# Performance work log

Measured on AMD Instinct MI355X. Metric: run time of the kernel, lower is better.

The kernel has to match this reference:

```python
import jax, jax.numpy as jnp
import numpy as np

Z, Y, X = 32, 480, 480          # sparse voxel grid (LiDAR-scale)
N = 200_000                     # active voxels
C_IN, C_OUT = 64, 64
EPS = 1e-5


def _subm_conv(f, nbr, w):
    """Submanifold sparse conv as gather-matmul-accumulate.
    f: [N, Cin]; nbr: [N, K] neighbor row ids, pad index == N for missing;
    w: [K, Cin, Cout]."""
    f_pad = jnp.concatenate([f, jnp.zeros((1, f.shape[1]), f.dtype)], axis=0)
    g = f_pad[nbr]                       # [N, K, Cin] gathered neighbor features
    return jnp.einsum('nkc,kco->no', g, w)


def _bn(x, gamma, beta):
    # BatchNorm1d in training mode: batch stats over the N dimension
    m = x.mean(axis=0)
    v = x.var(axis=0)
    return (x - m) * jax.lax.rsqrt(v + EPS) * gamma + beta


def setup_inputs() -> dict:
    rng = np.random.default_rng(0)
    ids = rng.choice(Z * Y * X, size=N, replace=False)
    lookup = np.full(Z * Y * X, -1, dtype=np.int64)
    lookup[ids] = np.arange(N)
    z = ids // (Y * X)
    y = (ids // X) % Y
    x = ids % X

    def nbr_table(offsets):
        cols = []
        for dz, dy, dx in offsets:
            zz, yy, xx = z + dz, y + dy, x + dx
            ok = (zz >= 0) & (zz < Z) & (yy >= 0) & (yy < Y) & (xx >= 0) & (xx < X)
            lin = np.clip((zz * Y + yy) * X + xx, 0, Z * Y * X - 1)
            idx = np.where(ok, lookup[lin], -1)
            cols.append(np.where(idx >= 0, idx, N))   # pad index N -> zero row
        return jnp.asarray(np.stack(cols, axis=1).astype(np.int32))

    off13 = [(0, dy, dx) for dy in (-1, 0, 1) for dx in (-1, 0, 1)]  # kernel (1,3,3)
    off31 = [(dz, 0, dx) for dz in (-1, 0, 1) for dx in (-1, 0, 1)]  # kernel (3,1,3)

    key = jax.random.key(0)
    ks = jax.random.split(key, 5)
    s = 0.05
    ones = jnp.ones((C_OUT,), jnp.float32)
    zeros = jnp.zeros((C_OUT,), jnp.float32)
    return {
        'features': jax.random.normal(ks[0], (N, C_IN), jnp.float32),
        'w1':   jax.random.normal(ks[1], (9, C_IN, C_OUT), jnp.float32) * s,
        'w1_2': jax.random.normal(ks[2], (9, C_OUT, C_OUT), jnp.float32) * s,
        'w2':   jax.random.normal(ks[3], (9, C_IN, C_OUT), jnp.float32) * s,
        'w3':   jax.random.normal(ks[4], (9, C_OUT, C_OUT), jnp.float32) * s,
        'g0': ones, 'b0': zeros, 'g0_2': ones, 'b0_2': zeros,
        'g1': ones, 'b1': zeros, 'g2': ones, 'b2': zeros,
        'nbr13': nbr_table(off13),
        'nbr31': nbr_table(off31),
    }


def reference(features, w1, w1_2, w2, w3, g0, b0, g0_2, b0_2, g1, b1, g2, b2,
              nbr13, nbr31):
    # shortcut branch: conv1x3 -> LeakyReLU -> BN -> conv3x1 -> LeakyReLU -> BN
    sc = _subm_conv(features, nbr13, w1)
    sc = _bn(jax.nn.leaky_relu(sc), g0, b0)
    sc = _subm_conv(sc, nbr31, w1_2)
    sc = _bn(jax.nn.leaky_relu(sc), g0_2, b0_2)
    # main branch: conv3x1 -> LeakyReLU -> BN -> conv1x3 -> LeakyReLU -> BN
    r = _subm_conv(features, nbr31, w2)
    r = _bn(jax.nn.leaky_relu(r), g1, b1)
    r = _subm_conv(r, nbr13, w3)
    r = _bn(jax.nn.leaky_relu(r), g2, b2)
    return r + sc
```

## Files before the change

kernel.cpp:

```cpp
#include <hip/hip_runtime.h>

#define NVOX 200000
#define TM 128
#define NBLK 1563
#define NREP 32
#define STG 4224

typedef unsigned short u16;
typedef unsigned int u32;
typedef __bf16 bf16x8 __attribute__((ext_vector_type(8)));
typedef float f32x16 __attribute__((ext_vector_type(16)));

__device__ __forceinline__ float bf2f(u16 h) { return __uint_as_float(((u32)h) << 16); }
__device__ __forceinline__ u16 f2bf(float x) {
  u32 u = __float_as_uint(x);
  u32 r = u + 0x7fffu + ((u >> 16) & 1u);
  return (u16)(r >> 16);
}
__device__ __forceinline__ uint4 cvt8(uint4 a, uint4 b) {
  const float* fa = (const float*)&a;
  const float* fb = (const float*)&b;
  uint4 r;
  u16* q = (u16*)&r;
#pragma unroll
  for (int j = 0; j < 4; ++j) { q[j] = f2bf(fa[j]); q[4 + j] = f2bf(fb[j]); }
  return r;
}
__device__ __forceinline__ int popnext(u32& m) {
  int k = __builtin_ctz(m); m &= m - 1; return k;
}

template <int PHASE>
__global__ __launch_bounds__(256, 4)
void conv_fused(const u16* __restrict__ inA, const u16* __restrict__ inB,
                const int* __restrict__ nbrA, const int* __restrict__ nbrB,
                const u16* __restrict__ wfA, const u16* __restrict__ wfB,
                const u16* __restrict__ zrow,
                void* yA, void* yB, float* __restrict__ stA, float* __restrict__ stB) {
  __shared__ __align__(16) float fb4[64 * 68];
  __shared__ float sred[4][128];

  const int tid = threadIdx.x;
  const int bid = blockIdx.x;
  const bool hB = (bid >= NBLK);
  const int blk = hB ? bid - NBLK : bid;
  const u16* f = hB ? inB : inA;
  const int* nbr = hB ? nbrB : nbrA;
  const u16* wf = hB ? wfB : wfA;
  float* st = hB ? stB : stA;

  const int wv = tid >> 6;
  const int lane = tid & 63;
  const int lrow = lane & 31;
  const int lq = lane >> 5;
  const int base = blk * TM;
  const int gr = base + wv * 32 + lrow;
  const bool okrow = (gr < NVOX);
  const int* nrow = nbr + (size_t)(okrow ? gr : 0) * 9;

  constexpr bool FOLDED = (PHASE == 1);
  constexpr int KSTRIDE = FOLDED ? 5120 : 4096;

  u32 live = 1u << 4;
  {
    int idt[9];
#pragma unroll
    for (int j = 0; j < 9; ++j) idt[j] = okrow ? nrow[j] : NVOX;
#pragma unroll
    for (int j = 0; j < 9; ++j)
      if (j != 4 && __ballot(idt[j] < NVOX) != 0ull) live |= 1u << j;
  }

  f32x16 acc0 = {0.f, 0.f, 0.f, 0.f, 0.f, 0.f, 0.f, 0.f,
                 0.f, 0.f, 0.f, 0.f, 0.f, 0.f, 0.f, 0.f};
  f32x16 acc1 = acc0;

  auto LDID = [&](int k) { return okrow ? nrow[k] : NVOX; };
  auto G = [&](uint4 (&d)[4], int id) {
    const u16* p = (id < NVOX) ? (f + (size_t)id * 64) : zrow;
    p += lq * 8;
    d[0] = *(const uint4*)(p);
    d[1] = *(const uint4*)(p + 16);
    d[2] = *(const uint4*)(p + 32);
    d[3] = *(const uint4*)(p + 48);
  };
  auto MMA = [&](const uint4 (&s)[4], int k, int id) {
    const u16* wb = wf + k * KSTRIDE;
#pragma unroll
    for (int ksi = 0; ksi < 4; ++ksi) {
      bf16x8 a = __builtin_bit_cast(bf16x8, s[ksi]);
      bf16x8 b0 = __builtin_bit_cast(bf16x8, *(const uint4*)(wb + (ksi * 2) * 512 + lane * 8));
      bf16x8 b1 = __builtin_bit_cast(bf16x8, *(const uint4*)(wb + (ksi * 2 + 1) * 512 + lane * 8));
      acc0 = __builtin_amdgcn_mfma_f32_32x32x16_bf16(a, b0, acc0, 0, 0, 0);
      acc1 = __builtin_amdgcn_mfma_f32_32x32x16_bf16(a, b1, acc1, 0, 0, 0);
    }
    if constexpr (FOLDED) {
      uint4 a4 = make_uint4(0u, 0u, 0u, 0u);
      if (lq == 0 && id < NVOX) ((u16*)&a4)[0] = 0x3F80u;
      bf16x8 a = __builtin_bit_cast(bf16x8, a4);
      bf16x8 b0 = __builtin_bit_cast(bf16x8, *(const uint4*)(wb + 8 * 512 + lane * 8));
      bf16x8 b1 = __builtin_bit_cast(bf16x8, *(const uint4*)(wb + 9 * 512 + lane * 8));
      acc0 = __builtin_amdgcn_mfma_f32_32x32x16_bf16(a, b0, acc0, 0, 0, 0);
      acc1 = __builtin_amdgcn_mfma_f32_32x32x16_bf16(a, b1, acc1, 0, 0, 0);
    }
  };

  {
    uint4 X[4], Y[4];
    int k0 = popnext(live);
    int id0 = LDID(k0);
    G(X, id0);
    while (true) {
      int k1 = -1, id1 = NVOX;
      if (live) { k1 = popnext(live); id1 = LDID(k1); G(Y, id1); }
      MMA(X, k0, id0);
      if (k1 < 0) break;
      int k2 = -1, id2 = NVOX;
      if (live) { k2 = popnext(live); id2 = LDID(k2); G(X, id2); }
      MMA(Y, k1, id1);
      if (k2 < 0) break;
      k0 = k2; id0 = id2;
    }
  }

  const int cc0 = lrow, cc1 = 32 + lrow;
  float s0 = 0.f, q0 = 0.f, s1 = 0.f, q1 = 0.f;
  float vout[2][16];
#pragma unroll
  for (int r = 0; r < 16; ++r) {
    float v = acc0[r]; v = v > 0.f ? v : 0.01f * v;
    s0 += v; q0 += v * v; vout[0][r] = v;
    float w = acc1[r]; w = w > 0.f ? w : 0.01f * w;
    s1 += w; q1 += w * w; vout[1][r] = w;
  }
  s0 += __shfl_xor(s0, 32); q0 += __shfl_xor(q0, 32);
  s1 += __shfl_xor(s1, 32); q1 += __shfl_xor(q1, 32);
  if (lq == 0) {
    sred[wv][lrow] = s0; sred[wv][32 + lrow] = s1;
    sred[wv][64 + lrow] = q0; sred[wv][96 + lrow] = q1;
  }

  const bool f32out = (PHASE == 1) && !hB;
  const int trow = tid >> 3, cp = tid & 7;
  u16* bb = (u16*)fb4;
#pragma unroll
  for (int h = 0; h < 2; ++h) {
    __syncthreads();
    if ((wv >> 1) == h) {
      const int lr = 32 * (wv & 1);
#pragma unroll
      for (int r = 0; r < 16; ++r) {
        int rowD = lr + (r & 3) + 8 * (r >> 2) + 4 * lq;
        if (f32out) {
          fb4[rowD * 68 + cc0] = vout[0][r];
          fb4[rowD * 68 + cc1] = vout[1][r];
        } else {
          bb[rowD * 72 + cc0] = f2bf(vout[0][r]);
          bb[rowD * 72 + cc1] = f2bf(vout[1][r]);
        }
      }
    }
    __syncthreads();
    if (f32out) {
      float* y = (float*)yA;
#pragma unroll
      for (int it = 0; it < 2; ++it) {
        int r = it * 32 + trow, row = base + 64 * h + r;
        if (row < NVOX) {
          *(float4*)(y + (size_t)row * 64 + cp * 8) = *(const float4*)(fb4 + r * 68 + cp * 8);
          *(float4*)(y + (size_t)row * 64 + cp * 8 + 4) = *(const float4*)(fb4 + r * 68 + cp * 8 + 4);
        }
      }
    } else {
      u16* y = (u16*)(hB ? yB : yA);
#pragma unroll
      for (int it = 0; it < 2; ++it) {
        int r = it * 32 + trow, row = base + 64 * h + r;
        if (row < NVOX)
          *(uint4*)(y + (size_t)row * 64 + cp * 8) = *(const uint4*)(bb + r * 72 + cp * 8);
      }
    }
  }
  if (tid < 128) {
    int which = tid >> 6, c = tid & 63;
    float v = sred[0][which * 64 + c] + sred[1][which * 64 + c] +
              sred[2][which * 64 + c] + sred[3][which * 64 + c];
    atomicAdd(&st[(bid & (NREP - 1)) * 128 + which * 64 + c], v);
  }
}

template <bool IN_F32, bool FOLDED, int MODE>
__global__ __launch_bounds__(256, 4)
void conv_k(const void* __restrict__ fv, const int* __restrict__ nbr,
            const u16* __restrict__ wf, void* yv, float* __restrict__ st,
            float* io, const float* __restrict__ affD,
            const float* __restrict__ affB) {
  __shared__ __align__(16) float fb[128 * 68];
  __shared__ float sred[4][128];

  const int tid = threadIdx.x;
  const int wv = tid >> 6;
  const int lane = tid & 63;
  const int lrow = lane & 31;
  const int lq = lane >> 5;
  const int base = blockIdx.x * TM;
  const int gr = base + wv * 32 + lrow;

  int ids[9];
#pragma unroll
  for (int j = 0; j < 9; ++j) ids[j] = (gr < NVOX) ? nbr[gr * 9 + j] : NVOX;

  f32x16 acc0 = {0.f, 0.f, 0.f, 0.f, 0.f, 0.f, 0.f, 0.f,
                 0.f, 0.f, 0.f, 0.f, 0.f, 0.f, 0.f, 0.f};
  f32x16 acc1 = acc0;
  constexpr int KSTRIDE = FOLDED ? 5120 : 4096;

#pragma unroll
  for (int k = 0; k < 9; ++k) {
    if (k != 4) {
      if (__ballot(ids[k] < NVOX) == 0ull) continue;
    }
    const int id = ids[k];
    const bool ok = id < NVOX;
    uint4 af[4];
    if constexpr (IN_F32) {
      const float* p = (const float*)fv + (size_t)id * 64 + lq * 8;
#pragma unroll
      for (int ksi = 0; ksi < 4; ++ksi) {
        uint4 v0 = make_uint4(0u, 0u, 0u, 0u), v1 = v0;
        if (ok) { v0 = *(const uint4*)(p + ksi * 16); v1 = *(const uint4*)(p + ksi * 16 + 4); }
        af[ksi] = cvt8(v0, v1);
      }
    } else {
      const u16* p = (const u16*)fv + (size_t)id * 64 + lq * 8;
#pragma unroll
      for (int ksi = 0; ksi < 4; ++ksi) {
        uint4 v = make_uint4(0u, 0u, 0u, 0u);
        if (ok) v = *(const uint4*)(p + ksi * 16);
        af[ksi] = v;
      }
    }
    const u16* wb = wf + k * KSTRIDE;
#pragma unroll
    for (int ksi = 0; ksi < 4; ++ksi) {
      bf16x8 a = __builtin_bit_cast(bf16x8, af[ksi]);
      bf16x8 b0 = __builtin_bit_cast(bf16x8, *(const uint4*)(wb + (ksi * 2) * 512 + lane * 8));
      bf16x8 b1 = __builtin_bit_cast(bf16x8, *(const uint4*)(wb + (ksi * 2 + 1) * 512 + lane * 8));
      acc0 = __builtin_amdgcn_mfma_f32_32x32x16_bf16(a, b0, acc0, 0, 0, 0);
      acc1 = __builtin_amdgcn_mfma_f32_32x32x16_bf16(a, b1, acc1, 0, 0, 0);
    }
    if constexpr (FOLDED) {
      uint4 a4 = make_uint4(0u, 0u, 0u, 0u);
      if (lq == 0 && ok) ((u16*)&a4)[0] = 0x3F80u;
      bf16x8 a = __builtin_bit_cast(bf16x8, a4);
      bf16x8 b0 = __builtin_bit_cast(bf16x8, *(const uint4*)(wb + 8 * 512 + lane * 8));
      bf16x8 b1 = __builtin_bit_cast(bf16x8, *(const uint4*)(wb + 9 * 512 + lane * 8));
      acc0 = __builtin_amdgcn_mfma_f32_32x32x16_bf16(a, b0, acc0, 0, 0, 0);
      acc1 = __builtin_amdgcn_mfma_f32_32x32x16_bf16(a, b1, acc1, 0, 0, 0);
    }
  }

  const int cc0 = lrow, cc1 = 32 + lrow;
  float aD0 = 0.f, aD1 = 0.f, hD0 = 0.f, hD1 = 0.f;
  if constexpr (MODE == 2) {
    aD0 = affD[cc0]; hD0 = affD[64 + cc0];
    aD1 = affD[cc1]; hD1 = affD[64 + cc1];
  }
  float s0 = 0.f, q0 = 0.f, s1 = 0.f, q1 = 0.f;
  float vout[2][16];
#pragma unroll
  for (int r = 0; r < 16; ++r) {
    float v = acc0[r]; v = v > 0.f ? v : 0.01f * v;
    s0 += v; q0 += v * v; vout[0][r] = v;
    float w = acc1[r]; w = w > 0.f ? w : 0.01f * w;
    s1 += w; q1 += w * w; vout[1][r] = w;
  }
  if constexpr (MODE != 2) {
    s0 += __shfl_xor(s0, 32); q0 += __shfl_xor(q0, 32);
    s1 += __shfl_xor(s1, 32); q1 += __shfl_xor(q1, 32);
    if (lq == 0) {
      sred[wv][lrow] = s0; sred[wv][32 + lrow] = s1;
      sred[wv][64 + lrow] = q0; sred[wv][96 + lrow] = q1;
    }
  }
  if constexpr (MODE == 0) {
    u16* bb = (u16*)fb;
#pragma unroll
    for (int r = 0; r < 16; ++r) {
      int rowD = 32 * wv + (r & 3) + 8 * (r >> 2) + 4 * lq;
      bb[rowD * 72 + cc0] = f2bf(vout[0][r]);
      bb[rowD * 72 + cc1] = f2bf(vout[1][r]);
    }
  } else if constexpr (MODE == 2 || MODE == 3) {
#pragma unroll
    for (int r = 0; r < 16; ++r) {
      int rowD = 32 * wv + (r & 3) + 8 * (r >> 2) + 4 * lq;
      float v0 = vout[0][r], v1 = vout[1][r];
      if constexpr (MODE == 2) { v0 = fmaf(v0, aD0, hD0); v1 = fmaf(v1, aD1, hD1); }
      fb[rowD * 68 + cc0] = v0;
      fb[rowD * 68 + cc1] = v1;
    }
  }
  __syncthreads();

  const int trow = tid >> 3, cp = tid & 7;
  if constexpr (MODE == 0) {
    u16* y = (u16*)yv;
    const u16* bb = (const u16*)fb;
#pragma unroll
    for (int it = 0; it < 4; ++it) {
      int r = it * 32 + trow, row = base + r;
      if (row < NVOX)
        *(uint4*)(y + (size_t)row * 64 + cp * 8) = *(const uint4*)(bb + r * 72 + cp * 8);
    }
  }
  if constexpr (MODE == 3) {
    float* y = (float*)yv;
#pragma unroll
    for (int it = 0; it < 4; ++it) {
      int r = it * 32 + trow, row = base + r;
      if (row < NVOX) {
        *(float4*)(y + (size_t)row * 64 + cp * 8) = *(const float4*)(fb + r * 68 + cp * 8);
        *(float4*)(y + (size_t)row * 64 + cp * 8 + 4) = *(const float4*)(fb + r * 68 + cp * 8 + 4);
      }
    }
  }
  if constexpr (MODE == 2) {
    float* y = (float*)yv;
#pragma unroll
    for (int it = 0; it < 4; ++it) {
      int r = it * 32 + trow, row = base + r;
      if (row < NVOX) {
        float t[8], p[8], o[8];
        *(float4*)&t[0] = *(const float4*)(fb + r * 68 + cp * 8);
        *(float4*)&t[4] = *(const float4*)(fb + r * 68 + cp * 8 + 4);
        *(float4*)&p[0] = *(const float4*)(io + (size_t)row * 64 + cp * 8);
        *(float4*)&p[4] = *(const float4*)(io + (size_t)row * 64 + cp * 8 + 4);
#pragma unroll
        for (int j = 0; j < 8; ++j) {
          int c = cp * 8 + j;
          o[j] = t[j] + fmaf(p[j], affB[c], affB[64 + c]);
        }
        *(float4*)(y + (size_t)row * 64 + cp * 8) = *(const float4*)&o[0];
        *(float4*)(y + (size_t)row * 64 + cp * 8 + 4) = *(const float4*)&o[4];
      }
    }
  }
  if constexpr (MODE != 2) {
    if (tid < 128) {
      int which = tid >> 6, c = tid & 63;
      float v = sred[0][which * 64 + c] + sred[1][which * 64 + c] +
                sred[2][which * 64 + c] + sred[3][which * 64 + c];
      atomicAdd(&st[(blockIdx.x & (NREP - 1)) * 128 + which * 64 + c], v);
    }
  }
}

__global__ void prep_all(const float* __restrict__ feat, const float* __restrict__ w1,
                         const float* __restrict__ w2, u16* __restrict__ wf,
                         u16* __restrict__ F, float* __restrict__ st,
                         u16* __restrict__ zr, int cvt_blocks) {
  const int bid = blockIdx.x, tid = threadIdx.x;
  if (bid < cvt_blocks) {
    int i8 = (bid * 256 + tid) * 8;
    if (i8 < NVOX * 64) {
      uint4 a = *(const uint4*)(feat + i8);
      uint4 b = *(const uint4*)(feat + i8 + 4);
      *(uint4*)(F + i8) = cvt8(a, b);
    }
    return;
  }
  int rb = bid - cvt_blocks;
  if (rb < 288) {
    int e = rb * 256 + tid;
    int slot = e / 36864, r = e % 36864;
    int k = r >> 12, rr = r & 4095;
    int frag = rr >> 9, lane = (rr >> 3) & 63, j = rr & 7;
    int ks = frag >> 1, ct = frag & 1;
    int cin = ks * 16 + (lane >> 5) * 8 + j;
    int cout = ct * 32 + (lane & 31);
    const float* src = slot ? w2 : w1;
    wf[e] = f2bf(src[k * 4096 + cin * 64 + cout]);
    return;
  }
  for (int i = tid; i < 4 * STG; i += 256) st[i] = 0.f;
  if (tid < 32) ((u32*)zr)[tid] = 0u;
}

__device__ __forceinline__ void bn_from_replicas(const float* stp, const float* g,
                                                 const float* b, int c,
                                                 float* sc, float* sh) {
  float s = 0.f, q = 0.f;
#pragma unroll
  for (int r = 0; r < NREP; ++r) {
    s += stp[r * 128 + c];
    q += stp[r * 128 + 64 + c];
  }
  const float invn = 1.0f / (float)NVOX;
  float mean = s * invn;
  float var = q * invn - mean * mean;
  float sca = g[c] * rsqrtf(var + 1e-5f);
  *sc = sca;
  *sh = b[c] - mean * sca;
}

__global__ void wscale2(const float* __restrict__ wA, float* __restrict__ stpA,
                        const float* __restrict__ gA, const float* __restrict__ bA,
                        u16* __restrict__ dA,
                        const float* __restrict__ wB, float* __restrict__ stpB,
                        const float* __restrict__ gB, const float* __restrict__ bB,
                        u16* __restrict__ dB) {
  __shared__ float sc[64], sh[64];
  const int tid = threadIdx.x;
  const bool hB = (blockIdx.x >= 180);
  const float* wraw = hB ? wB : wA;
  float* stp = hB ? stpB : stpA;
  const float* g = hB ? gB : gA;
  const float* b = hB ? bB : bA;
  u16* dst = hB ? dB : dA;
  const int blk = hB ? blockIdx.x - 180 : blockIdx.x;
  if (tid < 64) {
    float a, h;
    bn_from_replicas(stp, g, b, tid, &a, &h);
    sc[tid] = a; sh[tid] = h;
    if (blk == 0) { stp[NREP * 128 + tid] = a; stp[NREP * 128 + 64 + tid] = h; }
  }
  __syncthreads();
  int e = blk * 256 + tid;
  int k = e / 5120, r = e % 5120;
  int frag = r >> 9, lane = (r >> 3) & 63, j = r & 7;
  int ks = frag >> 1, ct = frag & 1;
  int cout = ct * 32 + (lane & 31);
  u16 val = 0;
  if (ks < 4) {
    int cin = ks * 16 + (lane >> 5) * 8 + j;
    val = f2bf(sc[cin] * wraw[k * 4096 + cin * 64 + cout]);
  } else if (((lane >> 5) == 0) && j == 0) {
    float acc = 0.f;
    for (int c = 0; c < 64; ++c) acc += sh[c] * wraw[k * 4096 + c * 64 + cout];
    val = f2bf(acc);
  }
  dst[e] = val;
}

__global__ void finalize2(float* __restrict__ stA, const float* __restrict__ gA,
                          const float* __restrict__ bA, float* __restrict__ stB,
                          const float* __restrict__ gB, const float* __restrict__ bB) {
  int t = threadIdx.x;
  float* stp = (t < 64) ? stA : stB;
  const float* g = (t < 64) ? gA : gB;
  const float* b = (t < 64) ? bA : bB;
  int c = t & 63;
  if (t < 128) {
    float a, h;
    bn_from_replicas(stp, g, b, c, &a, &h);
    stp[NREP * 128 + c] = a;
    stp[NREP * 128 + 64 + c] = h;
  }
}

__global__ void final_add(const u16* __restrict__ y3, float* io,
                          const float* __restrict__ affB, const float* __restrict__ affD) {
  int i8 = (blockIdx.x * 256 + threadIdx.x) * 8;
  if (i8 < NVOX * 64) {
    float a[8];
    *(float4*)&a[0] = *(const float4*)(io + i8);
    *(float4*)&a[4] = *(const float4*)(io + i8 + 4);
    uint4 vd = *(const uint4*)(y3 + i8);
    const u16* pd = (const u16*)&vd;
    int cb = i8 & 63;
    float o[8];
#pragma unroll
    for (int j = 0; j < 8; ++j) {
      int c = cb + j;
      o[j] = fmaf(a[j], affB[c], affB[64 + c]) + fmaf(bf2f(pd[j]), affD[c], affD[64 + c]);
    }
    *(float4*)(io + i8) = *(const float4*)&o[0];
    *(float4*)(io + i8 + 4) = *(const float4*)&o[4];
  }
}

__global__ void final_add2(const u16* __restrict__ y3, float* io,
                           float* __restrict__ stB, const float* __restrict__ gB,
                           const float* __restrict__ bB,
                           float* __restrict__ stD, const float* __restrict__ gD,
                           const float* __restrict__ bD) {
  __shared__ float aff[4][64];
  const int t = threadIdx.x;
  if (t < 128) {
    float a, h;
    if (t < 64) { bn_from_replicas(stB, gB, bB, t, &a, &h); aff[0][t] = a; aff[1][t] = h; }
    else { int c = t - 64; bn_from_replicas(stD, gD, bD, c, &a, &h); aff[2][c] = a; aff[3][c] = h; }
  }
  __syncthreads();
  int i8 = (blockIdx.x * 256 + t) * 8;
  if (i8 < NVOX * 64) {
    float a[8];
    *(float4*)&a[0] = *(const float4*)(io + i8);
    *(float4*)&a[4] = *(const float4*)(io + i8 + 4);
    uint4 vd = *(const uint4*)(y3 + i8);
    const u16* pd = (const u16*)&vd;
    int cb = i8 & 63;
    float o[8];
#pragma unroll
    for (int j = 0; j < 8; ++j) {
      int c = cb + j;
      o[j] = fmaf(a[j], aff[0][c], aff[1][c]) + fmaf(bf2f(pd[j]), aff[2][c], aff[3][c]);
    }
    *(float4*)(io + i8) = *(const float4*)&o[0];
    *(float4*)(io + i8 + 4) = *(const float4*)&o[4];
  }
}

extern "C" void kernel_launch(void* const* d_in, const int* in_sizes, int n_in,
                              void* d_out, int out_size, void* d_ws, size_t ws_size,
                              hipStream_t stream) {
  const float* feat = (const float*)d_in[0];
  const float* w1 = (const float*)d_in[1];
  const float* w1_2 = (const float*)d_in[2];
  const float* w2 = (const float*)d_in[3];
  const float* w3 = (const float*)d_in[4];
  const float* g0 = (const float*)d_in[5];
  const float* b0 = (const float*)d_in[6];
  const float* g0_2 = (const float*)d_in[7];
  const float* b0_2 = (const float*)d_in[8];
  const float* g1 = (const float*)d_in[9];
  const float* b1 = (const float*)d_in[10];
  const float* g2 = (const float*)d_in[11];
  const float* b2 = (const float*)d_in[12];
  const int* nbr13 = (const int*)d_in[13];
  const int* nbr31 = (const int*)d_in[14];
  float* out = (float*)d_out;

  char* ws = (char*)d_ws;
  float* st = (float*)ws;
  u16* wf = (u16*)(ws + 67584);
  u16* s0 = wf;
  u16* s1 = wf + 36864;
  u16* s2 = wf + 73728;
  u16* s3 = wf + 119808;
  u16* zr = (u16*)(ws + 399360);
  u16* F = (u16*)(ws + 399488);
  u16* A1 = F + (size_t)NVOX * 64;
  u16* A2 = A1 + (size_t)NVOX * 64;
  const size_t base_sz = 399488;
  const size_t need_fused = base_sz + 3ull * NVOX * 64 * 2;
  const size_t need_serial = base_sz + 2ull * NVOX * 64 * 2;

  float* st0 = st, *st1 = st + STG, *st2 = st + 2 * STG, *st3 = st + 3 * STG;

  if (ws_size >= need_fused) {
    prep_all<<<6539, 256, 0, stream>>>(feat, w1, w2, wf, F, st, zr, 6250);
    conv_fused<0><<<2 * NBLK, 256, 0, stream>>>(F, F, nbr13, nbr31, s0, s1, zr,
                                                A1, A2, st0, st2);
    wscale2<<<360, 256, 0, stream>>>(w1_2, st0, g0, b0, s2, w3, st2, g1, b1, s3);
    conv_fused<1><<<2 * NBLK, 256, 0, stream>>>(A1, A2, nbr31, nbr13, s2, s3, zr,
                                                out, F, st1, st3);
    final_add2<<<6250, 256, 0, stream>>>(F, out, st1, g0_2, b0_2, st3, g2, b2);
  } else if (ws_size >= need_serial) {
    prep_all<<<6539, 256, 0, stream>>>(feat, w1, w2, wf, F, st, zr, 6250);
    conv_k<false, false, 0><<<NBLK, 256, 0, stream>>>(F, nbr13, s0, A1, st0, nullptr, nullptr, nullptr);
    wscale2<<<180, 256, 0, stream>>>(w1_2, st0, g0, b0, s2, w3, st2, g1, b1, s3);
    conv_k<false, true, 3><<<NBLK, 256, 0, stream>>>(A1, nbr31, s2, out, st1, nullptr, nullptr, nullptr);
    conv_k<false, false, 0><<<NBLK, 256, 0, stream>>>(F, nbr31, s1, A1, st2, nullptr, nullptr, nullptr);
    wscale2<<<360, 256, 0, stream>>>(w1_2, st0, g0, b0, s2, w3, st2, g1, b1, s3);
    conv_k<false, true, 0><<<NBLK, 256, 0, stream>>>(A1, nbr13, s3, F, st3, nullptr, nullptr, nullptr);
    finalize2<<<1, 128, 0, stream>>>(st1, g0_2, b0_2, st3, g2, b2);
    final_add<<<6250, 256, 0, stream>>>(F, out, st1 + NREP * 128, st3 + NREP * 128);
  } else {
    u16* Az = F;
    prep_all<<<289, 256, 0, stream>>>(feat, w1, w2, wf, nullptr, st, zr, 0);
    conv_k<true, false, 0><<<NBLK, 256, 0, stream>>>(feat, nbr13, s0, Az, st0, nullptr, nullptr, nullptr);
    wscale2<<<180, 256, 0, stream>>>(w1_2, st0, g0, b0, s2, w3, st2, g1, b1, s3);
    conv_k<false, true, 3><<<NBLK, 256, 0, stream>>>(Az, nbr31, s2, out, st1, nullptr, nullptr, nullptr);
    finalize2<<<1, 128, 0, stream>>>(st1, g0_2, b0_2, st3, g2, b2);
    conv_k<true, false, 0><<<NBLK, 256, 0, stream>>>(feat, nbr31, s1, Az, st2, nullptr, nullptr, nullptr);
    wscale2<<<360, 256, 0, stream>>>(w1_2, st0, g0, b0, s2, w3, st2, g1, b1, s3);
    conv_k<false, true, 1><<<NBLK, 256, 0, stream>>>(Az, nbr13, s3, nullptr, st3, nullptr, nullptr, nullptr);
    finalize2<<<1, 128, 0, stream>>>(st1, g0_2, b0_2, st3, g2, b2);
    conv_k<false, true, 2><<<NBLK, 256, 0, stream>>>(Az, nbr13, s3, out, nullptr, out,
                                                     st3 + NREP * 128, st1 + NREP * 128);
  }
}
```

Baseline: 280.2 us.

## Stage conv weights in LDS with 512-thread blocks and a fixed tap loop

The fused conv kernel now uses 512 threads covering 256 rows. At the start of each block it copies all nine weight taps (72 KB) into shared memory, and the MFMA B operands are then read from LDS instead of global memory. The software-pipelined popcount tap loop is replaced by a fully unrolled loop over the nine taps that skips taps which are dead for the whole wave. The output store is reorganised into 16-row chunks using a small LDS buffer with a sync per chunk. This cuts repeated global weight reads and halves the block count, but the 72 KB of LDS per block may limit occupancy. It also adds 32 block-wide barriers and drops the explicit gather prefetch overlap.

Measured after the change: 275.7 us. About the same (-1.6%).

```diff
diff --git a/kernel.cpp b/kernel.cpp
--- a/kernel.cpp
+++ b/kernel.cpp
@@ -3,6 +3,7 @@
 #define NVOX 200000
 #define TM 128
 #define NBLK 1563
+#define NBLK8 782
 #define NREP 32
 #define STG 4224
 
@@ -26,69 +27,73 @@
   for (int j = 0; j < 4; ++j) { q[j] = f2bf(fa[j]); q[4 + j] = f2bf(fb[j]); }
   return r;
 }
-__device__ __forceinline__ int popnext(u32& m) {
-  int k = __builtin_ctz(m); m &= m - 1; return k;
-}
 
 template <int PHASE>
-__global__ __launch_bounds__(256, 4)
+__global__ __launch_bounds__(512, 4)
 void conv_fused(const u16* __restrict__ inA, const u16* __restrict__ inB,
                 const int* __restrict__ nbrA, const int* __restrict__ nbrB,
                 const u16* __restrict__ wfA, const u16* __restrict__ wfB,
                 const u16* __restrict__ zrow,
                 void* yA, void* yB, float* __restrict__ stA, float* __restrict__ stB) {
-  __shared__ __align__(16) float fb4[64 * 68];
-  __shared__ float sred[4][128];
+  __shared__ __align__(16) u16 wlds[9 * 4096];
+  __shared__ __align__(16) float fbx[16 * 68 + 8];
 
   const int tid = threadIdx.x;
   const int bid = blockIdx.x;
-  const bool hB = (bid >= NBLK);
-  const int blk = hB ? bid - NBLK : bid;
+  const bool hB = (bid >= NBLK8);
+  const int blk = hB ? bid - NBLK8 : bid;
   const u16* f = hB ? inB : inA;
   const int* nbr = hB ? nbrB : nbrA;
   const u16* wf = hB ? wfB : wfA;
   float* st = hB ? stB : stA;
 
+  constexpr bool FOLDED = (PHASE == 1);
+  constexpr int KSTRIDE = FOLDED ? 5120 : 4096;
+
+#pragma unroll
+  for (int j = 0; j < 9; ++j) {
+    int idx = j * 512 + tid;
+    int tap = idx >> 9;
+    int off = idx & 511;
+    *(uint4*)(wlds + tap * 4096 + off * 8) =
+        *(const uint4*)(wf + tap * KSTRIDE + off * 8);
+  }
+  __syncthreads();
+
   const int wv = tid >> 6;
   const int lane = tid & 63;
   const int lrow = lane & 31;
   const int lq = lane >> 5;
-  const int base = blk * TM;
+  const int base = blk * 256;
   const int gr = base + wv * 32 + lrow;
-  const bool okrow = (gr < NVOX);
-  const int* nrow = nbr + (size_t)(okrow ? gr : 0) * 9;
-
-  constexpr bool FOLDED = (PHASE == 1);
-  constexpr int KSTRIDE = FOLDED ? 5120 : 4096;
-
-  u32 live = 1u << 4;
-  {
-    int idt[9];
-#pragma unroll
-    for (int j = 0; j < 9; ++j) idt[j] = okrow ? nrow[j] : NVOX;
-#pragma unroll
-    for (int j = 0; j < 9; ++j)
-      if (j != 4 && __ballot(idt[j] < NVOX) != 0ull) live |= 1u << j;
-  }
+
+  int ids[9];
+#pragma unroll
+  for (int j = 0; j < 9; ++j) ids[j] = (gr < NVOX) ? nbr[gr * 9 + j] : NVOX;
 
   f32x16 acc0 = {0.f, 0.f, 0.f, 0.f, 0.f, 0.f, 0.f, 0.f,
                  0.f, 0.f, 0.f, 0.f, 0.f, 0.f, 0.f, 0.f};
   f32x16 acc1 = acc0;
 
-  auto LDID = [&](int k) { return okrow ? nrow[k] : NVOX; };
-  auto G = [&](uint4 (&d)[4], int id) {
-    const u16* p = (id < NVOX) ? (f + (size_t)id * 64) : zrow;
-    p += lq * 8;
-    d[0] = *(const uint4*)(p);
-    d[1] = *(const uint4*)(p + 16);
-    d[2] = *(const uint4*)(p + 32);
-    d[3] = *(const uint4*)(p + 48);
-  };
-  auto MMA = [&](const uint4 (&s)[4], int k, int id) {
-    const u16* wb = wf + k * KSTRIDE;
+#pragma unroll
+  for (int k = 0; k < 9; ++k) {
+    if (k != 4) {
+      if (__ballot(ids[k] < NVOX) == 0ull) continue;
+    }
+    const int id = ids[k];
+    const bool ok = id < NVOX;
+    uint4 af[4];
+    const u16* p = f + (size_t)id * 64 + lq * 8;
 #pragma unroll
     for (int ksi = 0; ksi < 4; ++ksi) {
-      bf16x8 a = __builtin_bit_cast(bf16x8, s[ksi]);
+      uint4 v = make_uint4(0u, 0u, 0u, 0u);
+      if (ok) v = *(const uint4*)(p + ksi * 16);
+      af[ksi] = v;
+    }
+    const u16* wb = wlds + k * 4096;
+#pragma unroll
+    for (int ksi = 0; ksi < 4; ++ksi) {
+      bf16x8 a = __builtin_bit_cast(bf16x8, af[ksi]);
       bf16x8 b0 = __builtin_bit_cast(bf16x8, *(const uint4*)(wb + (ksi * 2) * 512 + lane * 8));
       bf16x8 b1 = __builtin_bit_cast(bf16x8, *(const uint4*)(wb + (ksi * 2 + 1) * 512 + lane * 8));
       acc0 = __builtin_amdgcn_mfma_f32_32x32x16_bf16(a, b0, acc0, 0, 0, 0);
@@ -96,30 +101,13 @@
     }
     if constexpr (FOLDED) {
       uint4 a4 = make_uint4(0u, 0u, 0u, 0u);
-      if (lq == 0 && id < NVOX) ((u16*)&a4)[0] = 0x3F80u;
+      if (lq == 0 && ok) ((u16*)&a4)[0] = 0x3F80u;
       bf16x8 a = __builtin_bit_cast(bf16x8, a4);
-      bf16x8 b0 = __builtin_bit_cast(bf16x8, *(const uint4*)(wb + 8 * 512 + lane * 8));
-      bf16x8 b1 = __builtin_bit_cast(bf16x8, *(const uint4*)(wb + 9 * 512 + lane * 8));
+      const u16* wg = wf + k * KSTRIDE;
+      bf16x8 b0 = __builtin_bit_cast(bf16x8, *(const uint4*)(wg + 8 * 512 + lane * 8));
+      bf16x8 b1 = __builtin_bit_cast(bf16x8, *(const uint4*)(wg + 9 * 512 + lane * 8));
       acc0 = __builtin_amdgcn_mfma_f32_32x32x16_bf16(a, b0, acc0, 0, 0, 0);
       acc1 = __builtin_amdgcn_mfma_f32_32x32x16_bf16(a, b1, acc1, 0, 0, 0);
-    }
-  };
-
-  {
-    uint4 X[4], Y[4];
-    int k0 = popnext(live);
-    int id0 = LDID(k0);
-    G(X, id0);
-    while (true) {
-      int k1 = -1, id1 = NVOX;
-      if (live) { k1 = popnext(live); id1 = LDID(k1); G(Y, id1); }
-      MMA(X, k0, id0);
-      if (k1 < 0) break;
-      int k2 = -1, id2 = NVOX;
-      if (live) { k2 = popnext(live); id2 = LDID(k2); G(X, id2); }
-      MMA(Y, k1, id1);
-      if (k2 < 0) break;
-      k0 = k2; id0 = id2;
     }
   }
 
@@ -135,57 +123,60 @@
   }
   s0 += __shfl_xor(s0, 32); q0 += __shfl_xor(q0, 32);
   s1 += __shfl_xor(s1, 32); q1 += __shfl_xor(q1, 32);
+
+  float* sredf = fbx;
   if (lq == 0) {
-    sred[wv][lrow] = s0; sred[wv][32 + lrow] = s1;
-    sred[wv][64 + lrow] = q0; sred[wv][96 + lrow] = q1;
-  }
-
-  const bool f32out = (PHASE == 1) && !hB;
-  const int trow = tid >> 3, cp = tid & 7;
-  u16* bb = (u16*)fb4;
-#pragma unroll
-  for (int h = 0; h < 2; ++h) {
-    __syncthreads();
-    if ((wv >> 1) == h) {
-      const int lr = 32 * (wv & 1);
-#pragma unroll
-      for (int r = 0; r < 16; ++r) {
-        int rowD = lr + (r & 3) + 8 * (r >> 2) + 4 * lq;
-        if (f32out) {
-          fb4[rowD * 68 + cc0] = vout[0][r];
-          fb4[rowD * 68 + cc1] = vout[1][r];
-        } else {
-          bb[rowD * 72 + cc0] = f2bf(vout[0][r]);
-          bb[rowD * 72 + cc1] = f2bf(vout[1][r]);
-        }
-      }
-    }
-    __syncthreads();
-    if (f32out) {
-      float* y = (float*)yA;
-#pragma unroll
-      for (int it = 0; it < 2; ++it) {
-        int r = it * 32 + trow, row = base + 64 * h + r;
-        if (row < NVOX) {
-          *(float4*)(y + (size_t)row * 64 + cp * 8) = *(const float4*)(fb4 + r * 68 + cp * 8);
-          *(float4*)(y + (size_t)row * 64 + cp * 8 + 4) = *(const float4*)(fb4 + r * 68 + cp * 8 + 4);
-        }
-      }
-    } else {
-      u16* y = (u16*)(hB ? yB : yA);
-#pragma unroll
-      for (int it = 0; it < 2; ++it) {
-        int r = it * 32 + trow, row = base + 64 * h + r;
-        if (row < NVOX)
-          *(uint4*)(y + (size_t)row * 64 + cp * 8) = *(const uint4*)(bb + r * 72 + cp * 8);
-      }
-    }
-  }
+    sredf[wv * 128 + lrow] = s0;
+    sredf[wv * 128 + 32 + lrow] = s1;
+    sredf[wv * 128 + 64 + lrow] = q0;
+    sredf[wv * 128 + 96 + lrow] = q1;
+  }
+  __syncthreads();
   if (tid < 128) {
     int which = tid >> 6, c = tid & 63;
-    float v = sred[0][which * 64 + c] + sred[1][which * 64 + c] +
-              sred[2][which * 64 + c] + sred[3][which * 64 + c];
+    float v = 0.f;
+#pragma unroll
+    for (int w8 = 0; w8 < 8; ++w8) v += sredf[w8 * 128 + which * 64 + c];
     atomicAdd(&st[(bid & (NREP - 1)) * 128 + which * 64 + c], v);
+  }
+  __syncthreads();
+
+  const bool f32out = (PHASE == 1) && !hB;
+  float* yf = (float*)yA;
+  u16* yb = (u16*)(hB ? yB : yA);
+  u16* bbx = (u16*)fbx;
+#pragma unroll
+  for (int c = 0; c < 16; ++c) {
+    if (wv == (c >> 1)) {
+#pragma unroll
+      for (int rr = 0; rr < 8; ++rr) {
+        const int r = (c & 1) * 8 + rr;
+        const int row16 = (r & 3) + 8 * ((r >> 2) & 1) + 4 * lq;
+        if (f32out) {
+          fbx[row16 * 68 + cc0] = vout[0][r];
+          fbx[row16 * 68 + cc1] = vout[1][r];
+        } else {
+          bbx[row16 * 72 + cc0] = f2bf(vout[0][r]);
+          bbx[row16 * 72 + cc1] = f2bf(vout[1][r]);
+        }
+      }
+    }
+    __syncthreads();
+    const int row0 = base + c * 16;
+    if (f32out) {
+      if (tid < 256) {
+        int rr = tid >> 4, cp = tid & 15, row = row0 + rr;
+        if (row < NVOX)
+          *(float4*)(yf + (size_t)row * 64 + cp * 4) = *(const float4*)(fbx + rr * 68 + cp * 4);
+      }
+    } else {
+      if (tid < 128) {
+        int rr = tid >> 3, cp = tid & 7, row = row0 + rr;
+        if (row < NVOX)
+          *(uint4*)(yb + (size_t)row * 64 + cp * 8) = *(const uint4*)(bbx + rr * 72 + cp * 8);
+      }
+    }
+    __syncthreads();
   }
 }
 
@@ -551,11 +542,11 @@
 
   if (ws_size >= need_fused) {
     prep_all<<<6539, 256, 0, stream>>>(feat, w1, w2, wf, F, st, zr, 6250);
-    conv_fused<0><<<2 * NBLK, 256, 0, stream>>>(F, F, nbr13, nbr31, s0, s1, zr,
-                                                A1, A2, st0, st2);
+    conv_fused<0><<<2 * NBLK8, 512, 0, stream>>>(F, F, nbr13, nbr31, s0, s1, zr,
+                                                 A1, A2, st0, st2);
     wscale2<<<360, 256, 0, stream>>>(w1_2, st0, g0, b0, s2, w3, st2, g1, b1, s3);
-    conv_fused<1><<<2 * NBLK, 256, 0, stream>>>(A1, A2, nbr31, nbr13, s2, s3, zr,
-                                                out, F, st1, st3);
+    conv_fused<1><<<2 * NBLK8, 512, 0, stream>>>(A1, A2, nbr31, nbr13, s2, s3, zr,
+                                                 out, F, st1, st3);
     final_add2<<<6250, 256, 0, stream>>>(F, out, st1, g0_2, b0_2, st3, g2, b2);
   } else if (ws_size >= need_serial) {
     prep_all<<<6539, 256, 0, stream>>>(feat, w1, w2, wf, F, st, zr, 6250);
```
